# Performance work log

Measured on AMD Instinct MI355X. Metric: run time of the kernel, lower is better.

## Reference

```python
import jax, jax.numpy as jnp
import numpy as np
from jax import lax

B, S, D, K, H, NSLOT = 16, 128, 64, 64, 128, 96  # batch, seq/context, input, inter, hidden, slots


def setup_inputs() -> dict:
    key = jax.random.key(0)
    k = jax.random.split(key, 7)
    x_contexts = jax.random.normal(k[0], (B, S, D), jnp.float32)
    time_contexts = jax.random.randint(k[1], (B, S, S), 0, NSLOT + 1)
    dist_contexts = jax.random.randint(k[2], (B, S, S), 0, NSLOT + 1)
    context_masks = jax.random.randint(k[3], (B, S, S), 0, 2).astype(bool)
    # xavier-normal style init, matching nn.init.xavier_normal_ scales
    time_weights = jax.random.normal(k[4], (NSLOT + 1, D, K), jnp.float32) * (2.0 / (D + K)) ** 0.5
    dist_weights = jax.random.normal(k[5], (NSLOT + 1, K, H), jnp.float32) * (2.0 / (K + H)) ** 0.5
    hidden_weights = jax.random.normal(k[6], (H, H), jnp.float32) * (2.0 / (H + H)) ** 0.5
    return {"x_contexts": x_contexts, "time_contexts": time_contexts,
            "dist_contexts": dist_contexts, "context_masks": context_masks,
            "time_weights": time_weights, "dist_weights": dist_weights,
            "hidden_weights": hidden_weights}


def reference(x_contexts, time_contexts, dist_contexts, context_masks,
              time_weights, dist_weights, hidden_weights):
    # x_contexts: (B,S,D); *_contexts: (B,S,S) int; context_masks: (B,S,S) bool
    Bb, Ss, Dd = x_contexts.shape
    Hh = hidden_weights.shape[0]
    pos = jnp.arange(Ss)

    def step(h, xs):
        t_idx, d_idx, m, i = xs  # t_idx,d_idx,m: (B,S); i: step index
        # original slices context to :i+1; equivalent jit-friendly form: mask out j>i
        valid = m & (pos[None, :] <= i)  # (B,S)
        Tw = time_weights[t_idx]  # (B,S,D,K) gather
        Dw = dist_weights[d_idx]  # (B,S,K,H) gather
        # x @ (Tw @ Dw) reassociated as (x @ Tw) @ Dw to avoid (B,S,D,H) intermediate
        xt = jnp.einsum('bsd,bsdk->bsk', x_contexts, Tw)
        xc = jnp.einsum('bsk,bskh->bsh', xt, Dw)
        xc = jnp.where(valid[..., None], xc, 0.0).sum(axis=1)  # (B,H)
        h_new = jax.nn.sigmoid(xc + h @ hidden_weights)
        return h_new, h_new

    h0 = jnp.zeros((Bb, Hh), x_contexts.dtype)
    xs = (jnp.swapaxes(time_contexts, 0, 1),
          jnp.swapaxes(dist_contexts, 0, 1),
          jnp.swapaxes(context_masks, 0, 1),
          jnp.arange(Ss))
    hT, outs = lax.scan(step, h0, xs)
    # outputs: (B,S,H), final hidden with leading unsqueezed dim: (1,B,H)
    return jnp.swapaxes(outs, 0, 1), hT[None]
```

## Files before the change

### kernel.cpp

```cpp
#include <hip/hip_runtime.h>
#include <math.h>


#define B_ 16
#define S_ 128
#define D_ 64
#define K_ 64
#define H_ 128
#define NS 97
#define NB 128
#define MAXE 132096

#define XC_OFF 0
#define BH_T   262144
#define BH_D   (BH_T + NS * NB)
#define CNT_T  (BH_D + NS * NB)
#define CNT_D  (CNT_T + NS)
#define CNT_B  (CNT_D + NS)
#define OFF_T  (CNT_B + 2048)
#define OFF_D  (OFF_T + 98)
#define OFF_B  (OFF_D + 98)
#define ENT_T  291464
#define ENT_DX (ENT_T + MAXE)
#define ENT_DP (ENT_DX + MAXE)
#define XT16_OFF (ENT_DP + MAXE)
#define Y16_OFF  (XT16_OFF + MAXE * 32)
#define NEED_BYTES ((size_t)(Y16_OFF + (size_t)MAXE * 64) * 4)

typedef _Float16 h2_t __attribute__((ext_vector_type(2)));
typedef _Float16 f16x8 __attribute__((ext_vector_type(8)));
typedef float f32x4 __attribute__((ext_vector_type(4)));

#if __has_builtin(__builtin_amdgcn_fdot2)
#define FDOT2(a, b, c) __builtin_amdgcn_fdot2((a), (b), (c), false)
#else
#define FDOT2(a, b, c) ((c) + (float)(a)[0] * (float)(b)[0] + (float)(a)[1] * (float)(b)[1])
#endif


__global__ __launch_bounds__(256) void k_hist1(const int* __restrict__ tc,
                                               const int* __restrict__ dc,
                                               const int* __restrict__ mk,
                                               unsigned* wsi) {
    __shared__ unsigned ht[NS], hd[NS], hb[16];
    int tid = threadIdx.x, blk = blockIdx.x;
    if (tid < NS) { ht[tid] = 0; hd[tid] = 0; }
    if (tid < 16) hb[tid] = 0;
    __syncthreads();
    int base = blk * 2048;
    #pragma unroll
    for (int u = 0; u < 8; u++) {
        int idx = base + tid + u * 256;
        int i = (idx >> 7) & 127, j = idx & 127;
        if (j <= i && mk[idx] != 0) {
            atomicAdd(&ht[tc[idx]], 1u);
            atomicAdd(&hd[dc[idx]], 1u);
            atomicAdd(&hb[(idx >> 7) & 15], 1u);
        }
    }
    __syncthreads();
    if (tid < NS) {
        wsi[BH_T + tid * NB + blk] = ht[tid];
        wsi[BH_D + tid * NB + blk] = hd[tid];
    }
    if (tid < 16) wsi[CNT_B + blk * 16 + tid] = hb[tid];
}

template <int CH>
__device__ unsigned scan_region(unsigned* in, unsigned* out, int L, unsigned* s) {
    int tid = threadIdx.x;
    unsigned loc[CH], sum = 0;
    #pragma unroll
    for (int k = 0; k < CH; k++) {
        int idx = tid * CH + k;
        loc[k] = (idx < L) ? in[idx] : 0u;
        sum += loc[k];
    }
    s[tid] = sum;
    __syncthreads();
    for (int o = 1; o < 1024; o <<= 1) {
        unsigned a = (tid >= o) ? s[tid - o] : 0u;
        __syncthreads();
        s[tid] += a;
        __syncthreads();
    }
    unsigned total = s[1023];
    unsigned run = s[tid] - sum;
    __syncthreads();
    #pragma unroll
    for (int k = 0; k < CH; k++) {
        int idx = tid * CH + k;
        if (idx < L) { out[idx] = run; run += loc[k]; }
    }
    __syncthreads();
    return total;
}

__global__ __launch_bounds__(1024) void k_scan_all(unsigned* wsi) {
    __shared__ unsigned s[1024];
    int tid = threadIdx.x;

    unsigned totT = scan_region<13>(wsi + BH_T, wsi + BH_T, NS * NB, s);
    if (tid < NS) {
        unsigned b0 = wsi[BH_T + tid * NB];
        unsigned b1 = (tid < NS - 1) ? wsi[BH_T + (tid + 1) * NB] : totT;
        wsi[OFF_T + tid] = b0;
        wsi[CNT_T + tid] = b1 - b0;
    }
    if (tid == 0) wsi[OFF_T + NS] = totT;
    __syncthreads();

    unsigned totD = scan_region<13>(wsi + BH_D, wsi + BH_D, NS * NB, s);
    if (tid < NS) {
        unsigned b0 = wsi[BH_D + tid * NB];
        unsigned b1 = (tid < NS - 1) ? wsi[BH_D + (tid + 1) * NB] : totD;
        wsi[OFF_D + tid] = b0;
        wsi[CNT_D + tid] = b1 - b0;
    }
    if (tid == 0) wsi[OFF_D + NS] = totD;
    __syncthreads();

    unsigned totB = scan_region<2>(wsi + CNT_B, wsi + OFF_B, 2048, s);
    if (tid == 0) wsi[OFF_B + 2048] = totB;
}

__global__ __launch_bounds__(256) void k_scatter(const int* __restrict__ tc,
                                                 const int* __restrict__ dc,
                                                 const int* __restrict__ mk,
                                                 unsigned* wsi, int useY) {
    __shared__ unsigned ct[NS], cd[NS], cb[16];
    int tid = threadIdx.x, blk = blockIdx.x;
    if (tid < NS) {
        ct[tid] = wsi[BH_T + tid * NB + blk];
        cd[tid] = wsi[BH_D + tid * NB + blk];
    }
    if (tid < 16) cb[tid] = wsi[OFF_B + blk * 16 + tid];
    __syncthreads();
    int base = blk * 2048;
    #pragma unroll
    for (int u = 0; u < 8; u++) {
        int idx = base + tid + u * 256;
        int i = (idx >> 7) & 127, j = idx & 127, b = idx >> 14;
        if (j <= i && mk[idx] != 0) {
            unsigned t = (unsigned)tc[idx], d = (unsigned)dc[idx];
            unsigned tpos = atomicAdd(&ct[t], 1u);
            wsi[ENT_T + tpos] = (unsigned)b | ((unsigned)i << 4) | ((unsigned)j << 11)
                              | (t << 18) | (d << 25);
            unsigned dpos = atomicAdd(&cd[d], 1u);
            unsigned yp = useY ? atomicAdd(&cb[(idx >> 7) & 15], 1u) : (unsigned)(idx >> 7);
            wsi[ENT_DX + dpos] = tpos;
            wsi[ENT_DP + dpos] = yp;
        }
    }
}

__global__ __launch_bounds__(256) void k_phaseA(const float* __restrict__ x,
                                                const float* __restrict__ tw,
                                                unsigned* wsi, float* wsf) {
    int t = blockIdx.x, c = blockIdx.y;
    int rows = (int)wsi[CNT_T + t] - c * 128;
    if (rows <= 0) return;
    if (rows > 128) rows = 128;
    unsigned base = wsi[OFF_T + t] + c * 128;

    __shared__ float stw[4096];
    __shared__ float sx[8192];
    __shared__ unsigned ent[128];
    int tid = threadIdx.x;

    const float4* twg = (const float4*)(tw + t * 4096);
    float4* stw4 = (float4*)stw;
    #pragma unroll
    for (int q = 0; q < 4; q++) stw4[q * 256 + tid] = twg[q * 256 + tid];
    if (tid < 128) ent[tid] = (tid < rows) ? wsi[ENT_T + base + tid] : 0u;
    __syncthreads();

    int lane16 = tid & 15, rquot = tid >> 4;
    #pragma unroll
    for (int p = 0; p < 8; p++) {
        int r = p * 16 + rquot;
        float4 v = make_float4(0.f, 0.f, 0.f, 0.f);
        if (r < rows) {
            unsigned e = ent[r];
            int b = e & 15, j = (e >> 11) & 127;
            v = *(const float4*)(x + (b * S_ + j) * D_ + lane16 * 4);
        }
        int col4 = lane16 ^ (r & 15);
        float* dst = &sx[r * 64 + col4 * 4];
        dst[0] = v.x; dst[1] = v.y; dst[2] = v.z; dst[3] = v.w;
    }
    __syncthreads();

    int rgrp = tid & 15, cgrp = tid >> 4;
    float4 acc[8];
    #pragma unroll
    for (int i = 0; i < 8; i++) acc[i] = make_float4(0.f, 0.f, 0.f, 0.f);
    #pragma unroll 4
    for (int dd = 0; dd < 64; dd++) {
        float4 w = stw4[dd * 16 + cgrp];
        int s_idx = (((dd >> 2) ^ rgrp) << 2) + (dd & 3);
        #pragma unroll
        for (int i = 0; i < 8; i++) {
            float a = sx[(rgrp + 16 * i) * 64 + s_idx];
            acc[i].x += a * w.x; acc[i].y += a * w.y;
            acc[i].z += a * w.z; acc[i].w += a * w.w;
        }
    }
    _Float16* XT = (_Float16*)(wsf + XT16_OFF);
    #pragma unroll
    for (int i = 0; i < 8; i++) {
        int r = rgrp + 16 * i;
        if (r < rows) {
            union { _Float16 h[4]; double d64; } u;
            u.h[0] = (_Float16)acc[i].x; u.h[1] = (_Float16)acc[i].y;
            u.h[2] = (_Float16)acc[i].z; u.h[3] = (_Float16)acc[i].w;
            *(double*)&XT[(size_t)(base + r) * 64 + cgrp * 4] = u.d64;
        }
    }
}

__global__ __launch_bounds__(256) void k_phaseB(const float* __restrict__ dw,
                                                unsigned* wsi, float* wsf, int useY) {
    int d = blockIdx.x, c = blockIdx.y;
    int rows = (int)wsi[CNT_D + d] - c * 128;
    if (rows <= 0) return;
    if (rows > 128) rows = 128;
    unsigned base = wsi[OFF_D + d] + c * 128;

    __shared__ _Float16 sa[128 * 64];
    __shared__ _Float16 sb[64 * 128];
    __shared__ unsigned entx_s[128], entp_s[128];
    int tid = threadIdx.x;

    if (tid < 128) {
        entx_s[tid] = (tid < rows) ? wsi[ENT_DX + base + tid] : 0u;
        entp_s[tid] = (tid < rows) ? wsi[ENT_DP + base + tid] : 0u;
    }
    const float4* dwg = (const float4*)(dw + (size_t)d * 8192);
    #pragma unroll
    for (int q = 0; q < 8; q++) {
        float4 v = dwg[q * 256 + tid];
        union { _Float16 h[4]; double d64; } u;
        u.h[0] = (_Float16)v.x; u.h[1] = (_Float16)v.y;
        u.h[2] = (_Float16)v.z; u.h[3] = (_Float16)v.w;
        *(double*)&sb[(q * 256 + tid) * 4] = u.d64;
    }
    __syncthreads();

    {
        int r = tid >> 1, hh = tid & 1;
        const _Float16* XT = (const _Float16*)(wsf + XT16_OFF);
        const f16x8* src = (const f16x8*)(XT + (size_t)entx_s[r] * 64 + hh * 32);
        #pragma unroll
        for (int mm = 0; mm < 4; mm++) {
            f16x8 hv = {0, 0, 0, 0, 0, 0, 0, 0};
            if (r < rows) hv = src[mm];
            int chunk = hh * 4 + mm;
            *(f16x8*)&sa[r * 64 + (chunk ^ (r & 7)) * 8] = hv;
        }
    }
    __syncthreads();

    int w = tid >> 6, lane = tid & 63;
    int l15 = lane & 15, lg = lane >> 4;
    f16x8 bf[2][2];
    #pragma unroll
    for (int n = 0; n < 2; n++) {
        int col = w * 32 + n * 16 + l15;
        #pragma unroll
        for (int ks = 0; ks < 2; ks++) {
            int kb = ks * 32 + lg * 8;
            f16x8 t;
            #pragma unroll
            for (int e = 0; e < 8; e++) t[e] = sb[(kb + e) * 128 + col];
            bf[n][ks] = t;
        }
    }
    f32x4 acc[8][2];
    f32x4 z = {0.f, 0.f, 0.f, 0.f};
    #pragma unroll
    for (int m = 0; m < 8; m++) { acc[m][0] = z; acc[m][1] = z; }

    #pragma unroll
    for (int m = 0; m < 8; m++) {
        int row = m * 16 + l15;
        f16x8 a0 = *(f16x8*)&sa[row * 64 + ((lg) ^ (row & 7)) * 8];
        f16x8 a1 = *(f16x8*)&sa[row * 64 + ((4 + lg) ^ (row & 7)) * 8];
        #pragma unroll
        for (int n = 0; n < 2; n++) {
            acc[m][n] = __builtin_amdgcn_mfma_f32_16x16x32_f16(a0, bf[n][0], acc[m][n], 0, 0, 0);
            acc[m][n] = __builtin_amdgcn_mfma_f32_16x16x32_f16(a1, bf[n][1], acc[m][n], 0, 0, 0);
        }
    }

    if (useY) {
        _Float16* Y16 = (_Float16*)(wsf + Y16_OFF);
        #pragma unroll
        for (int m = 0; m < 8; m++) {
            #pragma unroll
            for (int reg = 0; reg < 4; reg++) {
                int row = m * 16 + lg * 4 + reg;
                if (row < rows) {
                    _Float16* p = Y16 + (size_t)entp_s[row] * 128 + w * 32 + l15;
                    p[0]  = (_Float16)acc[m][0][reg];
                    p[16] = (_Float16)acc[m][1][reg];
                }
            }
        }
    } else {
        float* XC = wsf + XC_OFF;
        #pragma unroll
        for (int m = 0; m < 8; m++) {
            #pragma unroll
            for (int reg = 0; reg < 4; reg++) {
                int row = m * 16 + lg * 4 + reg;
                if (row < rows) {
                    float* p = XC + (size_t)entp_s[row] * 128 + w * 32 + l15;
                    atomicAdd(p + 0,  acc[m][0][reg]);
                    atomicAdd(p + 16, acc[m][1][reg]);
                }
            }
        }
    }
}

__global__ __launch_bounds__(128) void k_reduce(unsigned* wsi, float* wsf) {
    int bi = blockIdx.x, tid = threadIdx.x;
    unsigned n = wsi[CNT_B + bi], off = wsi[OFF_B + bi];
    const _Float16* Yp = (const _Float16*)(wsf + Y16_OFF) + (size_t)off * 128 + tid;
    float a0 = 0.f, a1 = 0.f, a2 = 0.f, a3 = 0.f;
    unsigned e = 0;
    for (; e + 4 <= n; e += 4) {
        a0 += (float)Yp[(size_t)e * 128];
        a1 += (float)Yp[(size_t)(e + 1) * 128];
        a2 += (float)Yp[(size_t)(e + 2) * 128];
        a3 += (float)Yp[(size_t)(e + 3) * 128];
    }
    for (; e < n; e++) a0 += (float)Yp[(size_t)e * 128];
    wsf[XC_OFF + (size_t)bi * 128 + tid] = (a0 + a1) + (a2 + a3);
}

#define RSTEP(XCREG, IDX, CURB)                                                \
    {                                                                          \
        float xc_use = XCREG;                                                  \
        if (i + 4 + (IDX) < 128) XCREG = XC[(i + 4 + (IDX)) * 128];            \
        const float4* hb = (const float4*)&h16[CURB][0];                       \
        float a0 = 0.f, a1 = 0.f, a2 = 0.f, a3 = 0.f;                          \
        _Pragma("unroll")                                                      \
        for (int q = 0; q < 16; q++) {                                         \
            union { float4 f4; h2_t h2[4]; } u;                                \
            u.f4 = hb[q];                                                      \
            a0 = FDOT2(u.h2[0], w2[4 * q + 0], a0);                            \
            a1 = FDOT2(u.h2[1], w2[4 * q + 1], a1);                            \
            a2 = FDOT2(u.h2[2], w2[4 * q + 2], a2);                            \
            a3 = FDOT2(u.h2[3], w2[4 * q + 3], a3);                            \
        }                                                                      \
        float v = xc_use + (a0 + a1) + (a2 + a3);                              \
        v = 1.f / (1.f + __expf(-v));                                          \
        val = v;                                                               \
        ((_Float16*)&h16[(CURB) ^ 1][0])[col] = (_Float16)v;                   \
        out[(size_t)(b * 128 + i + (IDX)) * 128 + col] = v;                    \
        __syncthreads();                                                       \
    }

__global__ __launch_bounds__(128) void k_recur(const float* __restrict__ hw,
                                               const float* __restrict__ wsf,
                                               float* __restrict__ out) {
    int b = blockIdx.x;
    __shared__ h2_t h16[2][64];
    int tid = threadIdx.x;
    int lane = tid & 63, wv = tid >> 6;
    int col = wv * 64 + lane;

    h2_t w2[64];
    #pragma unroll
    for (int m = 0; m < 64; m++) {
        h2_t p;
        p[0] = (_Float16)hw[(2 * m) * 128 + col];
        p[1] = (_Float16)hw[(2 * m + 1) * 128 + col];
        w2[m] = p;
    }
    if (tid < 64) h16[0][tid] = (h2_t)(_Float16)0.f;
    __syncthreads();

    const float* XC = wsf + XC_OFF + (size_t)b * 128 * 128 + col;
    float xc0 = XC[0 * 128], xc1 = XC[1 * 128], xc2 = XC[2 * 128], xc3 = XC[3 * 128];
    float val = 0.f;
    for (int i = 0; i < 128; i += 4) {
        RSTEP(xc0, 0, 0)
        RSTEP(xc1, 1, 1)
        RSTEP(xc2, 2, 0)
        RSTEP(xc3, 3, 1)
    }
    out[(size_t)B_ * S_ * H_ + b * 128 + col] = val;
}

extern "C" void kernel_launch(void* const* d_in, const int* in_sizes, int n_in,
                              void* d_out, int out_size, void* d_ws, size_t ws_size,
                              hipStream_t stream) {
    const float* x  = (const float*)d_in[0];
    const int*   tc = (const int*)d_in[1];
    const int*   dc = (const int*)d_in[2];
    const int*   mk = (const int*)d_in[3];
    const float* tw = (const float*)d_in[4];
    const float* dw = (const float*)d_in[5];
    const float* hw = (const float*)d_in[6];
    float*    out = (float*)d_out;
    float*    wsf = (float*)d_ws;
    unsigned* wsi = (unsigned*)d_ws;
    char*     wsb = (char*)d_ws;

    int useY = (ws_size >= NEED_BYTES) ? 1 : 0;
    if (!useY)
        hipMemsetAsync(wsb, 0, (size_t)262144 * 4, stream);

    k_hist1<<<dim3(NB), dim3(256), 0, stream>>>(tc, dc, mk, wsi);
    k_scan_all<<<dim3(1), dim3(1024), 0, stream>>>(wsi);
    k_scatter<<<dim3(NB), dim3(256), 0, stream>>>(tc, dc, mk, wsi, useY);
    k_phaseA<<<dim3(NS, 16), dim3(256), 0, stream>>>(x, tw, wsi, wsf);
    k_phaseB<<<dim3(NS, 16), dim3(256), 0, stream>>>(dw, wsi, wsf, useY);
    if (useY) k_reduce<<<dim3(2048), dim3(128), 0, stream>>>(wsi, wsf);
    k_recur<<<dim3(16), dim3(128), 0, stream>>>(hw, wsf, out);
}
```

Before: 132.0 us.

## Use f16 MFMA in phaseA and merge the two offset scans into one

Result: slower. 163.4 us (+23.8%).

```diff
diff --git a/kernel.cpp b/kernel.cpp
--- a/kernel.cpp
+++ b/kernel.cpp
@@ -100,24 +100,19 @@
     __shared__ unsigned s[1024];
     int tid = threadIdx.x;
 
-    unsigned totT = scan_region<13>(wsi + BH_T, wsi + BH_T, NS * NB, s);
+    unsigned tot = scan_region<25>(wsi + BH_T, wsi + BH_T, 2 * NS * NB, s);
+    unsigned totT = wsi[BH_D];
     if (tid < NS) {
         unsigned b0 = wsi[BH_T + tid * NB];
         unsigned b1 = (tid < NS - 1) ? wsi[BH_T + (tid + 1) * NB] : totT;
         wsi[OFF_T + tid] = b0;
         wsi[CNT_T + tid] = b1 - b0;
-    }
-    if (tid == 0) wsi[OFF_T + NS] = totT;
-    __syncthreads();
-
-    unsigned totD = scan_region<13>(wsi + BH_D, wsi + BH_D, NS * NB, s);
-    if (tid < NS) {
-        unsigned b0 = wsi[BH_D + tid * NB];
-        unsigned b1 = (tid < NS - 1) ? wsi[BH_D + (tid + 1) * NB] : totD;
-        wsi[OFF_D + tid] = b0;
-        wsi[CNT_D + tid] = b1 - b0;
-    }
-    if (tid == 0) wsi[OFF_D + NS] = totD;
+        unsigned d0 = wsi[BH_D + tid * NB];
+        unsigned d1 = (tid < NS - 1) ? wsi[BH_D + (tid + 1) * NB] : tot;
+        wsi[OFF_D + tid] = d0 - totT;
+        wsi[CNT_D + tid] = d1 - d0;
+    }
+    if (tid == 0) { wsi[OFF_T + NS] = totT; wsi[OFF_D + NS] = tot - totT; }
     __syncthreads();
 
     unsigned totB = scan_region<2>(wsi + CNT_B, wsi + OFF_B, 2048, s);
@@ -130,9 +125,10 @@
                                                  unsigned* wsi, int useY) {
     __shared__ unsigned ct[NS], cd[NS], cb[16];
     int tid = threadIdx.x, blk = blockIdx.x;
+    unsigned totT = wsi[OFF_T + NS];
     if (tid < NS) {
         ct[tid] = wsi[BH_T + tid * NB + blk];
-        cd[tid] = wsi[BH_D + tid * NB + blk];
+        cd[tid] = wsi[BH_D + tid * NB + blk] - totT;
     }
     if (tid < 16) cb[tid] = wsi[OFF_B + blk * 16 + tid];
     __syncthreads();
@@ -163,58 +159,77 @@
     if (rows > 128) rows = 128;
     unsigned base = wsi[OFF_T + t] + c * 128;
 
-    __shared__ float stw[4096];
-    __shared__ float sx[8192];
+    __shared__ _Float16 sa[128 * 64];
+    __shared__ _Float16 sb[64 * 64];
     __shared__ unsigned ent[128];
     int tid = threadIdx.x;
 
+    if (tid < 128) ent[tid] = (tid < rows) ? wsi[ENT_T + base + tid] : 0u;
     const float4* twg = (const float4*)(tw + t * 4096);
-    float4* stw4 = (float4*)stw;
-    #pragma unroll
-    for (int q = 0; q < 4; q++) stw4[q * 256 + tid] = twg[q * 256 + tid];
-    if (tid < 128) ent[tid] = (tid < rows) ? wsi[ENT_T + base + tid] : 0u;
-    __syncthreads();
-
-    int lane16 = tid & 15, rquot = tid >> 4;
-    #pragma unroll
-    for (int p = 0; p < 8; p++) {
-        int r = p * 16 + rquot;
-        float4 v = make_float4(0.f, 0.f, 0.f, 0.f);
-        if (r < rows) {
-            unsigned e = ent[r];
-            int b = e & 15, j = (e >> 11) & 127;
-            v = *(const float4*)(x + (b * S_ + j) * D_ + lane16 * 4);
-        }
-        int col4 = lane16 ^ (r & 15);
-        float* dst = &sx[r * 64 + col4 * 4];
-        dst[0] = v.x; dst[1] = v.y; dst[2] = v.z; dst[3] = v.w;
-    }
-    __syncthreads();
-
-    int rgrp = tid & 15, cgrp = tid >> 4;
-    float4 acc[8];
-    #pragma unroll
-    for (int i = 0; i < 8; i++) acc[i] = make_float4(0.f, 0.f, 0.f, 0.f);
-    #pragma unroll 4
-    for (int dd = 0; dd < 64; dd++) {
-        float4 w = stw4[dd * 16 + cgrp];
-        int s_idx = (((dd >> 2) ^ rgrp) << 2) + (dd & 3);
-        #pragma unroll
-        for (int i = 0; i < 8; i++) {
-            float a = sx[(rgrp + 16 * i) * 64 + s_idx];
-            acc[i].x += a * w.x; acc[i].y += a * w.y;
-            acc[i].z += a * w.z; acc[i].w += a * w.w;
-        }
-    }
+    #pragma unroll
+    for (int q = 0; q < 4; q++) {
+        float4 v = twg[q * 256 + tid];
+        union { _Float16 h[4]; double d64; } u;
+        u.h[0] = (_Float16)v.x; u.h[1] = (_Float16)v.y;
+        u.h[2] = (_Float16)v.z; u.h[3] = (_Float16)v.w;
+        *(double*)&sb[(q * 256 + tid) * 4] = u.d64;
+    }
+    __syncthreads();
+
+    {
+        int r = tid >> 1, hh = tid & 1;
+        unsigned e = ent[r];
+        int b = e & 15, j = (e >> 11) & 127;
+        const float4* src = (const float4*)(x + (b * S_ + j) * D_ + hh * 32);
+        #pragma unroll
+        for (int mm = 0; mm < 4; mm++) {
+            f16x8 hv = {0, 0, 0, 0, 0, 0, 0, 0};
+            if (r < rows) {
+                float4 v0 = src[mm * 2], v1 = src[mm * 2 + 1];
+                hv[0] = (_Float16)v0.x; hv[1] = (_Float16)v0.y;
+                hv[2] = (_Float16)v0.z; hv[3] = (_Float16)v0.w;
+                hv[4] = (_Float16)v1.x; hv[5] = (_Float16)v1.y;
+                hv[6] = (_Float16)v1.z; hv[7] = (_Float16)v1.w;
+            }
+            int chunk = hh * 4 + mm;
+            *(f16x8*)&sa[r * 64 + (chunk ^ (r & 7)) * 8] = hv;
+        }
+    }
+    __syncthreads();
+
+    int w = tid >> 6, lane = tid & 63;
+    int l15 = lane & 15, lg = lane >> 4;
+    f16x8 bf[2];
+    #pragma unroll
+    for (int ks = 0; ks < 2; ks++) {
+        int kb = ks * 32 + lg * 8;
+        f16x8 tt;
+        #pragma unroll
+        for (int e = 0; e < 8; e++) tt[e] = sb[(kb + e) * 64 + w * 16 + l15];
+        bf[ks] = tt;
+    }
+    f32x4 acc[8];
+    f32x4 z = {0.f, 0.f, 0.f, 0.f};
+    #pragma unroll
+    for (int m = 0; m < 8; m++) acc[m] = z;
+
+    #pragma unroll
+    for (int m = 0; m < 8; m++) {
+        int row = m * 16 + l15;
+        f16x8 a0 = *(f16x8*)&sa[row * 64 + ((lg) ^ (row & 7)) * 8];
+        f16x8 a1 = *(f16x8*)&sa[row * 64 + ((4 + lg) ^ (row & 7)) * 8];
+        acc[m] = __builtin_amdgcn_mfma_f32_16x16x32_f16(a0, bf[0], acc[m], 0, 0, 0);
+        acc[m] = __builtin_amdgcn_mfma_f32_16x16x32_f16(a1, bf[1], acc[m], 0, 0, 0);
+    }
+
     _Float16* XT = (_Float16*)(wsf + XT16_OFF);
     #pragma unroll
-    for (int i = 0; i < 8; i++) {
-        int r = rgrp + 16 * i;
-        if (r < rows) {
-            union { _Float16 h[4]; double d64; } u;
-            u.h[0] = (_Float16)acc[i].x; u.h[1] = (_Float16)acc[i].y;
-            u.h[2] = (_Float16)acc[i].z; u.h[3] = (_Float16)acc[i].w;
-            *(double*)&XT[(size_t)(base + r) * 64 + cgrp * 4] = u.d64;
+    for (int m = 0; m < 8; m++) {
+        #pragma unroll
+        for (int reg = 0; reg < 4; reg++) {
+            int row = m * 16 + lg * 4 + reg;
+            if (row < rows)
+                XT[(size_t)(base + row) * 64 + w * 16 + l15] = (_Float16)acc[m][reg];
         }
     }
 }
```
